# Optimization experiments

Measured on AMD Instinct MI355X. Metric: run time of the kernel, lower is better.

Reference implementation:

```python
import jax, jax.numpy as jnp
import numpy as np

D = 500  # hidden width hard-coded in the module

def _lrelu(x):
    # nn.LeakyReLU default negative_slope = 0.01
    return jnp.where(x > 0, x, 0.01 * x)

def setup_inputs() -> dict:
    key = jax.random.key(0)
    ks = jax.random.split(key, 20)
    T, B = 2048, 64
    inp = {
        "pitches": jax.random.normal(ks[0], (T, B, 128), dtype=jnp.float32),
        "velocities": jax.random.normal(ks[1], (T, B, 128), dtype=jnp.float32),
        "durations": jax.random.uniform(ks[2], (T, B, 1), dtype=jnp.float32),
        "steps": jax.random.uniform(ks[3], (T, B, 1), dtype=jnp.float32),
        # learned params (torch Linear convention: W is [out, in])
        "Wp": jax.random.normal(ks[4], (D, 128), dtype=jnp.float32) * 0.05,
        "bp": jax.random.normal(ks[5], (D,), dtype=jnp.float32) * 0.05,
        "Wv": jax.random.normal(ks[6], (D, 128), dtype=jnp.float32) * 0.05,
        "bv": jax.random.normal(ks[7], (D,), dtype=jnp.float32) * 0.05,
        "Wd": jax.random.normal(ks[8], (D, 1), dtype=jnp.float32) * 0.05,
        "bd": jax.random.normal(ks[9], (D,), dtype=jnp.float32) * 0.05,
        "Ws": jax.random.normal(ks[10], (D, 1), dtype=jnp.float32) * 0.05,
        "bs": jax.random.normal(ks[11], (D,), dtype=jnp.float32) * 0.05,
        "W1": jax.random.normal(ks[12], (D, D), dtype=jnp.float32) * 0.05,
        "b1": jax.random.normal(ks[13], (D,), dtype=jnp.float32) * 0.05,
        "W2": jax.random.normal(ks[14], (D, D), dtype=jnp.float32) * 0.05,
        "b2": jax.random.normal(ks[15], (D,), dtype=jnp.float32) * 0.05,
        "Wi": jax.random.normal(ks[16], (D, D), dtype=jnp.float32) * 0.05,
        "bi": jax.random.normal(ks[17], (D,), dtype=jnp.float32) * 0.05,
        "W3": jax.random.normal(ks[18], (1, D), dtype=jnp.float32) * 0.05,
        "b3": jax.random.normal(ks[19], (1,), dtype=jnp.float32) * 0.05,
    }
    return inp

def reference(pitches, velocities, durations, steps,
              Wp, bp, Wv, bv, Wd, bd, Ws, bs,
              W1, b1, W2, b2, Wi, bi, W3, b3):
    # Note: in the original torch code the LSTMCell output is computed then
    # discarded (overwritten), and `info` at step t depends only on inputs at
    # step t. Thus the final output depends only on the last timestep through
    # the embed-sum -> LeakyReLU MLP -> linear_intermediate chain.
    # Vectorized over all T timesteps (same per-step math as the loop body).
    add = (jnp.einsum('tbi,oi->tbo', pitches, Wp) + bp
           + jnp.einsum('tbi,oi->tbo', velocities, Wv) + bv
           + jnp.einsum('tbi,oi->tbo', durations, Wd) + bd
           + jnp.einsum('tbi,oi->tbo', steps, Ws) + bs)      # [T,B,500]
    h = _lrelu(jnp.einsum('tbi,oi->tbo', add, W1) + b1)
    h = _lrelu(jnp.einsum('tbi,oi->tbo', h, W2) + b2)
    info = jnp.einsum('tbi,oi->tbo', h, Wi) + bi              # [T,B,500]
    out = jax.nn.sigmoid(info[-1] @ W3.T + b3)                # [B,1]
    return out
```

## Files before the change

### kernel.cpp

```cpp
#include <hip/hip_runtime.h>

#define DD 500
#define BB 64
#define TT 2048
#define KP 128
#define VCHUNKS 32
#define VPSTRIDE 512

__global__ __launch_bounds__(256) void k_embed(
    const float* __restrict__ pitches, const float* __restrict__ velocities,
    const float* __restrict__ durations, const float* __restrict__ steps,
    const float* __restrict__ Wp, const float* __restrict__ bp,
    const float* __restrict__ Wv, const float* __restrict__ bv,
    const float* __restrict__ Wd, const float* __restrict__ bd,
    const float* __restrict__ Wst, const float* __restrict__ bs,
    float* __restrict__ addT)
{
    const int tid = threadIdx.x;
    const int bid = blockIdx.x;

    __shared__ float lds[KP * BB];
    const int b = tid & 63;
    const int o = __builtin_amdgcn_readfirstlane(bid * 4 + (tid >> 6));
    const float* __restrict__ wp = Wp + o * KP;
    const float* __restrict__ wv = Wv + o * KP;

    float a0 = 0.f, a1 = 0.f, a2 = 0.f, a3 = 0.f;

    const float4* Psrc = (const float4*)(pitches + (size_t)(TT - 1) * BB * KP);
    const float4* Vsrc = (const float4*)(velocities + (size_t)(TT - 1) * BB * KP);

    for (int j = tid; j < BB * KP / 4; j += 256) {
        float4 p = Psrc[j];
        int pb = j >> 5;
        int k0 = (j & 31) * 4;
        lds[(k0 + 0) * BB + ((pb + k0 + 0) & 63)] = p.x;
        lds[(k0 + 1) * BB + ((pb + k0 + 1) & 63)] = p.y;
        lds[(k0 + 2) * BB + ((pb + k0 + 2) & 63)] = p.z;
        lds[(k0 + 3) * BB + ((pb + k0 + 3) & 63)] = p.w;
    }
    __syncthreads();
    for (int k = 0; k < KP; k += 4) {
        a0 += lds[(k + 0) * BB + ((b + k + 0) & 63)] * wp[k + 0];
        a1 += lds[(k + 1) * BB + ((b + k + 1) & 63)] * wp[k + 1];
        a2 += lds[(k + 2) * BB + ((b + k + 2) & 63)] * wp[k + 2];
        a3 += lds[(k + 3) * BB + ((b + k + 3) & 63)] * wp[k + 3];
    }
    __syncthreads();

    for (int j = tid; j < BB * KP / 4; j += 256) {
        float4 p = Vsrc[j];
        int pb = j >> 5;
        int k0 = (j & 31) * 4;
        lds[(k0 + 0) * BB + ((pb + k0 + 0) & 63)] = p.x;
        lds[(k0 + 1) * BB + ((pb + k0 + 1) & 63)] = p.y;
        lds[(k0 + 2) * BB + ((pb + k0 + 2) & 63)] = p.z;
        lds[(k0 + 3) * BB + ((pb + k0 + 3) & 63)] = p.w;
    }
    __syncthreads();
    for (int k = 0; k < KP; k += 4) {
        a0 += lds[(k + 0) * BB + ((b + k + 0) & 63)] * wv[k + 0];
        a1 += lds[(k + 1) * BB + ((b + k + 1) & 63)] * wv[k + 1];
        a2 += lds[(k + 2) * BB + ((b + k + 2) & 63)] * wv[k + 2];
        a3 += lds[(k + 3) * BB + ((b + k + 3) & 63)] * wv[k + 3];
    }

    const float dur = durations[(size_t)(TT - 1) * BB + b];
    const float st  = steps[(size_t)(TT - 1) * BB + b];
    const float acc = bp[o] + bv[o] + bd[o] + bs[o]
                    + dur * Wd[o] + st * Wst[o]
                    + (a0 + a1) + (a2 + a3);
    addT[o * BB + b] = acc;
}

__global__ __launch_bounds__(256) void k_dense(
    const float* __restrict__ Ain, const float* __restrict__ W,
    const float* __restrict__ bias, float* __restrict__ Aout, int leaky,
    const float* __restrict__ Wi, const float* __restrict__ W3,
    float* __restrict__ vpart)
{
    const int tid = threadIdx.x;
    const int bid = blockIdx.x;

    if (bid >= DD) {
        const int oc = bid - DD;
        const int obeg = oc * 16;
        const int k0 = tid;
        const int k1 = tid + 256;
        float acc0 = 0.f, acc1 = 0.f;
        #pragma unroll
        for (int i = 0; i < 16; ++i) {
            const int o = obeg + i;
            const int oc_ = o < DD ? o : DD - 1;
            const float ww = o < DD ? W3[oc_] : 0.f;
            acc0 += ww * Wi[(size_t)oc_ * DD + k0];
            if (k1 < DD) acc1 += ww * Wi[(size_t)oc_ * DD + k1];
        }
        vpart[oc * VPSTRIDE + k0] = acc0;
        if (k1 < DD) vpart[oc * VPSTRIDE + k1] = acc1;
        return;
    }

    __shared__ float partial[4][BB];
    const int b = tid & 63;
    const int w = tid >> 6;
    const int o = bid;
    const float* __restrict__ wrow = W + o * DD;
    const int kbeg = w * 125;

    float a0 = 0.f, a1 = 0.f, a2 = 0.f, a3 = 0.f;
    float a4 = 0.f, a5 = 0.f, a6 = 0.f, a7 = 0.f;
    #pragma unroll 3
    for (int k = kbeg; k < kbeg + 120; k += 8) {
        a0 += Ain[(k + 0) * BB + b] * wrow[k + 0];
        a1 += Ain[(k + 1) * BB + b] * wrow[k + 1];
        a2 += Ain[(k + 2) * BB + b] * wrow[k + 2];
        a3 += Ain[(k + 3) * BB + b] * wrow[k + 3];
        a4 += Ain[(k + 4) * BB + b] * wrow[k + 4];
        a5 += Ain[(k + 5) * BB + b] * wrow[k + 5];
        a6 += Ain[(k + 6) * BB + b] * wrow[k + 6];
        a7 += Ain[(k + 7) * BB + b] * wrow[k + 7];
    }
    {
        const int k = kbeg + 120;
        a0 += Ain[(k + 0) * BB + b] * wrow[k + 0];
        a1 += Ain[(k + 1) * BB + b] * wrow[k + 1];
        a2 += Ain[(k + 2) * BB + b] * wrow[k + 2];
        a3 += Ain[(k + 3) * BB + b] * wrow[k + 3];
        a4 += Ain[(k + 4) * BB + b] * wrow[k + 4];
    }
    partial[w][b] = ((a0 + a1) + (a2 + a3)) + ((a4 + a5) + (a6 + a7));
    __syncthreads();
    if (w == 0) {
        float acc = bias[o] + (partial[0][b] + partial[1][b])
                            + (partial[2][b] + partial[3][b]);
        if (leaky) acc = acc > 0.f ? acc : 0.01f * acc;
        Aout[o * BB + b] = acc;
    }
}

__global__ __launch_bounds__(1024) void k_out(
    const float* __restrict__ h2T, const float* __restrict__ vpart,
    const float* __restrict__ W3, const float* __restrict__ bi,
    const float* __restrict__ b3, float* __restrict__ out)
{
    __shared__ float vv[DD];
    __shared__ float partial[16][BB];
    const int tid = threadIdx.x;

    if (tid < DD) {
        const int k = tid;
        float s0 = 0.f, s1 = 0.f, s2 = 0.f, s3 = 0.f;
        float s4 = 0.f, s5 = 0.f, s6 = 0.f, s7 = 0.f;
        #pragma unroll
        for (int oc = 0; oc < VCHUNKS; oc += 8) {
            s0 += vpart[(oc + 0) * VPSTRIDE + k];
            s1 += vpart[(oc + 1) * VPSTRIDE + k];
            s2 += vpart[(oc + 2) * VPSTRIDE + k];
            s3 += vpart[(oc + 3) * VPSTRIDE + k];
            s4 += vpart[(oc + 4) * VPSTRIDE + k];
            s5 += vpart[(oc + 5) * VPSTRIDE + k];
            s6 += vpart[(oc + 6) * VPSTRIDE + k];
            s7 += vpart[(oc + 7) * VPSTRIDE + k];
        }
        vv[k] = ((s0 + s1) + (s2 + s3)) + ((s4 + s5) + (s6 + s7));
    }
    __syncthreads();

    const int b = tid & 63;
    const int w = tid >> 6;
    const int kbeg = w * 32;
    const int kend = kbeg + 32 < DD ? kbeg + 32 : DD;

    float accA = 0.f, accB = 0.f, accC = 0.f, accD = 0.f;
    for (int k = kbeg; k < kend; k += 4) {
        accA += h2T[(k + 0) * BB + b] * vv[k + 0];
        accB += h2T[(k + 1) * BB + b] * vv[k + 1];
        accC += h2T[(k + 2) * BB + b] * vv[k + 2];
        accD += h2T[(k + 3) * BB + b] * vv[k + 3];
        accA += W3[k + 0] * bi[k + 0];
        accB += W3[k + 1] * bi[k + 1];
        accC += W3[k + 2] * bi[k + 2];
        accD += W3[k + 3] * bi[k + 3];
    }
    partial[w][b] = (accA + accB) + (accC + accD);
    __syncthreads();
    if (w == 0) {
        float s = b3[0];
        #pragma unroll
        for (int i = 0; i < 16; ++i) s += partial[i][b];
        out[b] = 1.f / (1.f + __expf(-s));
    }
}

extern "C" void kernel_launch(void* const* d_in, const int* in_sizes, int n_in,
                              void* d_out, int out_size, void* d_ws, size_t ws_size,
                              hipStream_t stream)
{
    const float* pitches    = (const float*)d_in[0];
    const float* velocities = (const float*)d_in[1];
    const float* durations  = (const float*)d_in[2];
    const float* steps      = (const float*)d_in[3];
    const float* Wp  = (const float*)d_in[4];
    const float* bp  = (const float*)d_in[5];
    const float* Wv  = (const float*)d_in[6];
    const float* bv  = (const float*)d_in[7];
    const float* Wd  = (const float*)d_in[8];
    const float* bd  = (const float*)d_in[9];
    const float* Wst = (const float*)d_in[10];
    const float* bs  = (const float*)d_in[11];
    const float* W1  = (const float*)d_in[12];
    const float* b1  = (const float*)d_in[13];
    const float* W2  = (const float*)d_in[14];
    const float* b2  = (const float*)d_in[15];
    const float* Wi  = (const float*)d_in[16];
    const float* bi  = (const float*)d_in[17];
    const float* W3  = (const float*)d_in[18];
    const float* b3  = (const float*)d_in[19];

    float* ws    = (float*)d_ws;
    float* addT  = ws;
    float* h1T   = ws + 32000;
    float* h2T   = ws + 64000;
    float* vpart = ws + 96000;

    float* out = (float*)d_out;

    k_embed<<<125, 256, 0, stream>>>(pitches, velocities, durations, steps,
                                     Wp, bp, Wv, bv, Wd, bd, Wst, bs, addT);
    k_dense<<<DD + VCHUNKS, 256, 0, stream>>>(addT, W1, b1, h1T, 1,
                                              Wi, W3, vpart);
    k_dense<<<DD, 256, 0, stream>>>(h1T, W2, b2, h2T, 1, Wi, W3, vpart);
    k_out<<<1, 1024, 0, stream>>>(h2T, vpart, W3, bi, b3, out);
}
```

Before: 191.2 us.

## Fuse final output kernel into second dense layer via last-block atomic counter

Merges the single-block output kernel into the second dense layer kernel. Each block publishes its h2 row with a threadfence and bumps an atomic counter, and the last block to finish reduces vpart and computes the sigmoid output. The counter is reset by the first dense kernel. This removes one kernel launch and its dependency gap, but the final reduction now runs on 256 threads instead of 1024 and adds atomic and fence overhead.

```diff
diff --git a/kernel.cpp b/kernel.cpp
--- a/kernel.cpp
+++ b/kernel.cpp
@@ -67,22 +67,22 @@
 
     const float dur = durations[(size_t)(TT - 1) * BB + b];
     const float st  = steps[(size_t)(TT - 1) * BB + b];
-    const float acc = bp[o] + bv[o] + bd[o] + bs[o]
-                    + dur * Wd[o] + st * Wst[o]
-                    + (a0 + a1) + (a2 + a3);
-    addT[o * BB + b] = acc;
-}
-
-__global__ __launch_bounds__(256) void k_dense(
+    addT[o * BB + b] = bp[o] + bv[o] + bd[o] + bs[o]
+                     + dur * Wd[o] + st * Wst[o]
+                     + (a0 + a1) + (a2 + a3);
+}
+
+__global__ __launch_bounds__(256) void k_dense1(
     const float* __restrict__ Ain, const float* __restrict__ W,
-    const float* __restrict__ bias, float* __restrict__ Aout, int leaky,
+    const float* __restrict__ bias, float* __restrict__ Aout,
     const float* __restrict__ Wi, const float* __restrict__ W3,
-    float* __restrict__ vpart)
+    float* __restrict__ vpart, int* __restrict__ counter)
 {
     const int tid = threadIdx.x;
     const int bid = blockIdx.x;
 
     if (bid >= DD) {
+        if (bid == DD && tid == 0) *counter = 0;
         const int oc = bid - DD;
         const int obeg = oc * 16;
         const int k0 = tid;
@@ -104,8 +104,7 @@
     __shared__ float partial[4][BB];
     const int b = tid & 63;
     const int w = tid >> 6;
-    const int o = bid;
-    const float* __restrict__ wrow = W + o * DD;
+    const float* __restrict__ wrow = W + bid * DD;
     const int kbeg = w * 125;
 
     float a0 = 0.f, a1 = 0.f, a2 = 0.f, a3 = 0.f;
@@ -132,24 +131,70 @@
     partial[w][b] = ((a0 + a1) + (a2 + a3)) + ((a4 + a5) + (a6 + a7));
     __syncthreads();
     if (w == 0) {
-        float acc = bias[o] + (partial[0][b] + partial[1][b])
-                            + (partial[2][b] + partial[3][b]);
-        if (leaky) acc = acc > 0.f ? acc : 0.01f * acc;
-        Aout[o * BB + b] = acc;
-    }
-}
-
-__global__ __launch_bounds__(1024) void k_out(
-    const float* __restrict__ h2T, const float* __restrict__ vpart,
-    const float* __restrict__ W3, const float* __restrict__ bi,
-    const float* __restrict__ b3, float* __restrict__ out)
-{
+        float acc = bias[bid] + (partial[0][b] + partial[1][b])
+                              + (partial[2][b] + partial[3][b]);
+        acc = acc > 0.f ? acc : 0.01f * acc;
+        Aout[bid * BB + b] = acc;
+    }
+}
+
+__global__ __launch_bounds__(256) void k_dense2_out(
+    const float* __restrict__ Ain, const float* __restrict__ W,
+    const float* __restrict__ bias, float* __restrict__ h2T,
+    const float* __restrict__ vpart, const float* __restrict__ W3,
+    const float* __restrict__ bi, const float* __restrict__ b3,
+    float* __restrict__ out, int* __restrict__ counter)
+{
+    __shared__ float partial[4][BB];
     __shared__ float vv[DD];
-    __shared__ float partial[16][BB];
+    __shared__ int isLast;
     const int tid = threadIdx.x;
-
-    if (tid < DD) {
-        const int k = tid;
+    const int bid = blockIdx.x;
+    const int b = tid & 63;
+    const int w = tid >> 6;
+    const float* __restrict__ wrow = W + bid * DD;
+    const int kbeg = w * 125;
+
+    float a0 = 0.f, a1 = 0.f, a2 = 0.f, a3 = 0.f;
+    float a4 = 0.f, a5 = 0.f, a6 = 0.f, a7 = 0.f;
+    #pragma unroll 3
+    for (int k = kbeg; k < kbeg + 120; k += 8) {
+        a0 += Ain[(k + 0) * BB + b] * wrow[k + 0];
+        a1 += Ain[(k + 1) * BB + b] * wrow[k + 1];
+        a2 += Ain[(k + 2) * BB + b] * wrow[k + 2];
+        a3 += Ain[(k + 3) * BB + b] * wrow[k + 3];
+        a4 += Ain[(k + 4) * BB + b] * wrow[k + 4];
+        a5 += Ain[(k + 5) * BB + b] * wrow[k + 5];
+        a6 += Ain[(k + 6) * BB + b] * wrow[k + 6];
+        a7 += Ain[(k + 7) * BB + b] * wrow[k + 7];
+    }
+    {
+        const int k = kbeg + 120;
+        a0 += Ain[(k + 0) * BB + b] * wrow[k + 0];
+        a1 += Ain[(k + 1) * BB + b] * wrow[k + 1];
+        a2 += Ain[(k + 2) * BB + b] * wrow[k + 2];
+        a3 += Ain[(k + 3) * BB + b] * wrow[k + 3];
+        a4 += Ain[(k + 4) * BB + b] * wrow[k + 4];
+    }
+    partial[w][b] = ((a0 + a1) + (a2 + a3)) + ((a4 + a5) + (a6 + a7));
+    __syncthreads();
+    if (w == 0) {
+        float acc = bias[bid] + (partial[0][b] + partial[1][b])
+                              + (partial[2][b] + partial[3][b]);
+        acc = acc > 0.f ? acc : 0.01f * acc;
+        h2T[bid * BB + b] = acc;
+        __threadfence();
+    }
+    __syncthreads();
+    if (tid == 0) {
+        int old = atomicAdd(counter, 1);
+        isLast = (old == DD - 1);
+    }
+    __syncthreads();
+    if (!isLast) return;
+    __threadfence();
+
+    for (int k = tid; k < DD; k += 256) {
         float s0 = 0.f, s1 = 0.f, s2 = 0.f, s3 = 0.f;
         float s4 = 0.f, s5 = 0.f, s6 = 0.f, s7 = 0.f;
         #pragma unroll
@@ -167,28 +212,24 @@
     }
     __syncthreads();
 
-    const int b = tid & 63;
-    const int w = tid >> 6;
-    const int kbeg = w * 32;
-    const int kend = kbeg + 32 < DD ? kbeg + 32 : DD;
-
-    float accA = 0.f, accB = 0.f, accC = 0.f, accD = 0.f;
-    for (int k = kbeg; k < kend; k += 4) {
-        accA += h2T[(k + 0) * BB + b] * vv[k + 0];
-        accB += h2T[(k + 1) * BB + b] * vv[k + 1];
-        accC += h2T[(k + 2) * BB + b] * vv[k + 2];
-        accD += h2T[(k + 3) * BB + b] * vv[k + 3];
-        accA += W3[k + 0] * bi[k + 0];
-        accB += W3[k + 1] * bi[k + 1];
-        accC += W3[k + 2] * bi[k + 2];
-        accD += W3[k + 3] * bi[k + 3];
-    }
-    partial[w][b] = (accA + accB) + (accC + accD);
+    {
+        float p0 = 0.f, p1 = 0.f, p2 = 0.f, p3 = 0.f;
+        for (int k = kbeg; k < kbeg + 124; k += 4) {
+            p0 += h2T[(k + 0) * BB + b] * vv[k + 0] + W3[k + 0] * bi[k + 0];
+            p1 += h2T[(k + 1) * BB + b] * vv[k + 1] + W3[k + 1] * bi[k + 1];
+            p2 += h2T[(k + 2) * BB + b] * vv[k + 2] + W3[k + 2] * bi[k + 2];
+            p3 += h2T[(k + 3) * BB + b] * vv[k + 3] + W3[k + 3] * bi[k + 3];
+        }
+        {
+            const int k = kbeg + 124;
+            p0 += h2T[k * BB + b] * vv[k] + W3[k] * bi[k];
+        }
+        partial[w][b] = (p0 + p1) + (p2 + p3);
+    }
     __syncthreads();
     if (w == 0) {
-        float s = b3[0];
-        #pragma unroll
-        for (int i = 0; i < 16; ++i) s += partial[i][b];
+        float s = b3[0] + (partial[0][b] + partial[1][b])
+                        + (partial[2][b] + partial[3][b]);
         out[b] = 1.f / (1.f + __expf(-s));
     }
 }
@@ -223,13 +264,14 @@
     float* h1T   = ws + 32000;
     float* h2T   = ws + 64000;
     float* vpart = ws + 96000;
+    int*   counter = (int*)(ws + 96000 + VCHUNKS * VPSTRIDE);
 
     float* out = (float*)d_out;
 
     k_embed<<<125, 256, 0, stream>>>(pitches, velocities, durations, steps,
                                      Wp, bp, Wv, bv, Wd, bd, Wst, bs, addT);
-    k_dense<<<DD + VCHUNKS, 256, 0, stream>>>(addT, W1, b1, h1T, 1,
-                                              Wi, W3, vpart);
-    k_dense<<<DD, 256, 0, stream>>>(h1T, W2, b2, h2T, 1, Wi, W3, vpart);
-    k_out<<<1, 1024, 0, stream>>>(h2T, vpart, W3, bi, b3, out);
-}
+    k_dense1<<<DD + VCHUNKS, 256, 0, stream>>>(addT, W1, b1, h1T,
+                                               Wi, W3, vpart, counter);
+    k_dense2_out<<<DD, 256, 0, stream>>>(h1T, W2, b2, h2T,
+                                         vpart, W3, bi, b3, out, counter);
+}
```

Result: slower. 202.2 us (+5.8%).
